# Performance work log

Measured on AMD Instinct MI355X. Metric: run time of the kernel, lower is better.

The kernel has to match this reference:

```python
import jax, jax.numpy as jnp
import numpy as np

N_E = 8192
E_DIM = 512
BETA = 0.25


def setup_inputs() -> dict:
    key = jax.random.key(0)
    k1, k2, k3, k4 = jax.random.split(key, 4)
    x = jax.random.normal(k1, (32, 512, E_DIM), dtype=jnp.float32)
    label = jax.random.randint(k2, (32, 512), 0, 100, dtype=jnp.int64)
    idx = jax.random.randint(k3, (32, 512), 0, 512, dtype=jnp.int64)
    # codebook initialized uniform(-1/n_e, 1/n_e) as in the torch module
    W = jax.random.uniform(k4, (N_E, E_DIM), dtype=jnp.float32,
                           minval=-1.0 / N_E, maxval=1.0 / N_E)
    return {"x": x, "label": label, "idx": idx, "W": W}


def reference(x, label, idx, W):
    # label/idx are unused in the forward math (mirrors the torch module)
    latent = x.reshape(-1, E_DIM)                        # [N, e_dim]
    # squared euclidean distances: ||z||^2 + ||c||^2 - 2 z c^T
    d = (jnp.sum(latent ** 2, axis=1, keepdims=True)
         + jnp.sum(W ** 2, axis=1)[None, :]
         - 2.0 * jnp.matmul(latent, W.T))                # [N, n_e]
    indices = jnp.argmin(d, axis=-1)                     # [N]
    x_q = W[indices].reshape(x.shape)                    # gather + reshape
    commitment_loss = jnp.mean((jax.lax.stop_gradient(x_q) - x) ** 2)
    loss = BETA * commitment_loss
    # straight-through estimator
    x_q = x + jax.lax.stop_gradient(x_q - x)
    indices = indices.reshape(x.shape[:-1])
    return x_q, loss, indices
```

## Files before the change

kernel.cpp:

```cpp
#include <hip/hip_runtime.h>
#include <cstdint>
#include <cstddef>

#define EDIM  512
#define NROWS 16384
#define NE    8192
#define XQSZ  (NROWS * EDIM)
#define NTILE 64
#define K3    1536

#define OFF_PART  0
#define OFF_Z     16384
#define OFF_C2    81920
#define OFF_KEYS  114688
#define OFF_TMIN  245760
#define OFF_CNT   4440064
#define OFF_LIST  4441088
#define OFF_XE    8635392
#define OFF_WE    58967040

typedef __attribute__((ext_vector_type(8)))  short          short8;
typedef __attribute__((ext_vector_type(16))) float          f32x16;
typedef __attribute__((ext_vector_type(4)))  unsigned short u16x4;

__device__ __forceinline__ float rownorm512(const float* __restrict__ p) {
#pragma clang fp contract(off)
    float S[4];
#pragma unroll
    for (int b = 0; b < 4; ++b) {
        const float* q = p + b * 128;
        float r[8];
#pragma unroll
        for (int j = 0; j < 8; ++j) { float v = q[j]; r[j] = v * v; }
        for (int i = 8; i < 128; i += 8) {
#pragma unroll
            for (int j = 0; j < 8; ++j) { float v = q[i + j]; r[j] = r[j] + v * v; }
        }
        S[b] = ((r[0] + r[1]) + (r[2] + r[3])) + ((r[4] + r[5]) + (r[6] + r[7]));
    }
    return (S[0] + S[1]) + (S[2] + S[3]);
}

__device__ __forceinline__ unsigned short f2bf(float f) {
    unsigned u = __float_as_uint(f);
    return (unsigned short)((u + 0x7FFFu + ((u >> 16) & 1u)) >> 16);
}
__device__ __forceinline__ float bf2f(unsigned short h) {
    return __uint_as_float(((unsigned)h) << 16);
}

__device__ __forceinline__ void split_group(const float* __restrict__ in,
        unsigned short* __restrict__ outp, int e) {
    int row = e >> 7;
    int d0  = (e & 127) << 2;
    float4 v = *(const float4*)(in + (size_t)row * EDIM + d0);
    float vv[4] = {v.x, v.y, v.z, v.w};
    u16x4 H, M, L;
#pragma unroll
    for (int i = 0; i < 4; ++i) {
        float f = vv[i];
        unsigned short h = f2bf(f);
        float r1 = f - bf2f(h);
        unsigned short m = f2bf(r1);
        float r2 = r1 - bf2f(m);
        L[i] = f2bf(r2); H[i] = h; M[i] = m;
    }
    unsigned short* o = outp + (size_t)row * K3 + d0;
    *(u16x4*)(o) = H; *(u16x4*)(o + EDIM) = M; *(u16x4*)(o + 2 * EDIM) = L;
}

__global__ __launch_bounds__(256) void k_prep(
        const float* __restrict__ x, const float* __restrict__ W,
        unsigned short* __restrict__ Xe, unsigned short* __restrict__ We,
        float* __restrict__ Z, float* __restrict__ c2) {
    const int bid = blockIdx.x, tid = threadIdx.x;
    if (bid < 8192) {
        split_group(x, Xe, bid * 256 + tid);
    } else if (bid < 12288) {
        split_group(W, We, (bid - 8192) * 256 + tid);
    } else if (bid < 12352) {
        const int row = (bid - 12288) * 256 + tid;
        Z[row] = rownorm512(x + (size_t)row * EDIM);
    } else {
        const int row = (bid - 12352) * 256 + tid;
        c2[row] = rownorm512(W + (size_t)row * EDIM);
    }
}

__device__ __forceinline__ void gld16(const void* g, void* l) {
    __builtin_amdgcn_global_load_lds((const __attribute__((address_space(1))) void*)g,
                                     (__attribute__((address_space(3))) void*)l, 16, 0, 0);
}

#define GBM 128
#define GBN 128
#define GBK 64

__global__ __launch_bounds__(256) void k_argmin_hi(
        const unsigned short* __restrict__ Xe, const unsigned short* __restrict__ We,
        const float* __restrict__ c2, unsigned* __restrict__ tmin) {
    __shared__ __align__(16) unsigned short At[GBM * GBK];
    __shared__ __align__(16) unsigned short Bt[GBN * GBK];
    __shared__ unsigned smin[GBM];
    __shared__ float cs[GBN];

    const int tid = threadIdx.x;
    const int lane = tid & 63, wid = tid >> 6;
    const int wr = wid >> 1, wc = wid & 1;

    const int bid = blockIdx.x;
    const int swz = (bid & 7) * 1024 + (bid >> 3);
    const int rowtile = swz & 127, codetile = swz >> 7;
    const int row0 = rowtile * GBM, code0 = codetile * GBN;

    if (tid < GBM) smin[tid] = 0xFFFFFFFFu;
    if (tid < GBN) cs[tid] = 4.0f + c2[code0 + tid];

    f32x16 acc[2][2];
#pragma unroll
    for (int i = 0; i < 2; ++i)
#pragma unroll
        for (int j = 0; j < 2; ++j)
#pragma unroll
            for (int r = 0; r < 16; ++r) acc[i][j][r] = 0.0f;

    size_t ga[4], gb[4];
#pragma unroll
    for (int i = 0; i < 4; ++i) {
        int chunk = i * 256 + tid;
        int row   = chunk >> 3;
        int kcs   = (chunk & 7) ^ (row & 7);
        ga[i] = (size_t)(row0 + row) * K3 + kcs * 8;
        gb[i] = (size_t)(code0 + row) * K3 + kcs * 8;
    }

    const int cb0 = wr * 64 + (lane & 31);
    const int xa0 = wc * 64 + (lane & 31);
    const int kh  = lane >> 5;
    const int sb  = cb0 & 7, sa = xa0 & 7;

    for (int kt = 0; kt < EDIM / GBK; ++kt) {
        const size_t ko = (size_t)kt * GBK;
#pragma unroll
        for (int i = 0; i < 4; ++i) {
            gld16(Xe + ga[i] + ko, (char*)At + i * 4096 + wid * 1024);
            gld16(We + gb[i] + ko, (char*)Bt + i * 4096 + wid * 1024);
        }
        __syncthreads();
#pragma unroll
        for (int ks = 0; ks < 4; ++ks) {
            const int ch = ks * 2 + kh;
            short8 c0 = *(const short8*)((const char*)Bt + cb0 * 128        + ((ch ^ sb) * 16));
            short8 c1 = *(const short8*)((const char*)Bt + (cb0 + 32) * 128 + ((ch ^ sb) * 16));
            short8 x0 = *(const short8*)((const char*)At + xa0 * 128        + ((ch ^ sa) * 16));
            short8 x1 = *(const short8*)((const char*)At + (xa0 + 32) * 128 + ((ch ^ sa) * 16));
            acc[0][0] = __builtin_amdgcn_mfma_f32_32x32x16_bf16(c0, x0, acc[0][0], 0, 0, 0);
            acc[0][1] = __builtin_amdgcn_mfma_f32_32x32x16_bf16(c0, x1, acc[0][1], 0, 0, 0);
            acc[1][0] = __builtin_amdgcn_mfma_f32_32x32x16_bf16(c1, x0, acc[1][0], 0, 0, 0);
            acc[1][1] = __builtin_amdgcn_mfma_f32_32x32x16_bf16(c1, x1, acc[1][1], 0, 0, 0);
        }
        __syncthreads();
    }

    const int kh4 = kh * 4;
#pragma unroll
    for (int nj = 0; nj < 2; ++nj) {
        float dmin = 3.4e38f;
#pragma unroll
        for (int mi = 0; mi < 2; ++mi) {
#pragma unroll
            for (int q = 0; q < 4; ++q) {
                const float4 cq = *(const float4*)&cs[wr * 64 + mi * 32 + q * 8 + kh4];
                dmin = fminf(dmin, fmaf(-2.0f, acc[mi][nj][q * 4 + 0], cq.x));
                dmin = fminf(dmin, fmaf(-2.0f, acc[mi][nj][q * 4 + 1], cq.y));
                dmin = fminf(dmin, fmaf(-2.0f, acc[mi][nj][q * 4 + 2], cq.z));
                dmin = fminf(dmin, fmaf(-2.0f, acc[mi][nj][q * 4 + 3], cq.w));
            }
        }
        const int xr = wc * 64 + nj * 32 + (lane & 31);
        atomicMin(&smin[xr], __float_as_uint(dmin));
    }
    __syncthreads();
    if (tid < GBM) tmin[codetile * NROWS + row0 + tid] = smin[tid];
}

__global__ __launch_bounds__(256) void k_select(
        const unsigned* __restrict__ tmin, const float* __restrict__ Z,
        int* __restrict__ cnt, int* __restrict__ list) {
    const int row = blockIdx.x * 256 + threadIdx.x;
    unsigned mn = 0xFFFFFFFFu;
    for (int t = 0; t < NTILE; ++t) {
        unsigned v = tmin[t * NROWS + row];
        if (v < mn) mn = v;
    }
    const float margin = 4.35e-5f * sqrtf(Z[row]) + 1.7e-4f;
    const float thr = __uint_as_float(mn) + margin;
    for (int t = 0; t < NTILE; ++t) {
        if (__uint_as_float(tmin[t * NROWS + row]) <= thr) {
            int p = atomicAdd(&cnt[t], 1);
            list[t * NROWS + p] = row;
        }
    }
}

__global__ __launch_bounds__(256) void k_rescore_mfma(
        const unsigned short* __restrict__ Xe, const unsigned short* __restrict__ We,
        const float* __restrict__ Z, const float* __restrict__ c2,
        const int* __restrict__ cnt, const int* __restrict__ list,
        unsigned long long* __restrict__ keys) {
    __shared__ __align__(16) unsigned short At[2][GBM * GBK];
    __shared__ __align__(16) unsigned short Bt[2][GBN * GBK];
    __shared__ int rl_s[GBM];
    __shared__ float Zs[GBM];
    __shared__ float cs2[GBN];

    const int tile = blockIdx.x;
    const int n = cnt[tile];
    if (n == 0) return;
    const int* rows = list + tile * NROWS;
    const int tid = threadIdx.x;
    const int lane = tid & 63, wid = tid >> 6;
    const int wr = wid >> 1, wc = wid & 1;
    const int code0 = tile * 128;

    if (tid < GBN) cs2[tid] = c2[code0 + tid];

    const int cb0 = wr * 64 + (lane & 31);
    const int xa0 = wc * 64 + (lane & 31);
    const int kh  = lane >> 5;
    const int kh4 = kh * 4;
    const int sb  = cb0 & 7, sa = xa0 & 7;

    size_t boff[4];
    int arow4[4], akcs4[4];
#pragma unroll
    for (int i = 0; i < 4; ++i) {
        int chunk = i * 256 + tid;
        int row   = chunk >> 3;
        int kcs   = (chunk & 7) ^ (row & 7);
        arow4[i] = row; akcs4[i] = kcs;
        boff[i] = (size_t)(code0 + row) * K3 + kcs * 8;
    }

#define RSTAGE(ss, bb) { \
        const int bt_ = (ss) >> 3, kc_ = (ss) & 7; \
        const int ao_ = (bt_ == 1 || bt_ == 2) ? EDIM : (bt_ == 4 ? 2 * EDIM : 0); \
        const int bo_ = (bt_ == 0 || bt_ == 2) ? EDIM : (bt_ == 3 ? 2 * EDIM : 0); \
        _Pragma("unroll") \
        for (int i_ = 0; i_ < 4; ++i_) { \
            gld16(Xe + aoff[i_] + ao_ + kc_ * GBK, (char*)At[bb] + i_ * 4096 + wid * 1024); \
            gld16(We + boff[i_] + bo_ + kc_ * GBK, (char*)Bt[bb] + i_ * 4096 + wid * 1024); \
        } }

#define RCOMP(bb) { \
        _Pragma("unroll") \
        for (int ks_ = 0; ks_ < 4; ++ks_) { \
            const int ch_ = ks_ * 2 + kh; \
            short8 cf0 = *(const short8*)((const char*)Bt[bb] + cb0 * 128        + ((ch_ ^ sb) * 16)); \
            short8 cf1 = *(const short8*)((const char*)Bt[bb] + (cb0 + 32) * 128 + ((ch_ ^ sb) * 16)); \
            short8 xf0 = *(const short8*)((const char*)At[bb] + xa0 * 128        + ((ch_ ^ sa) * 16)); \
            short8 xf1 = *(const short8*)((const char*)At[bb] + (xa0 + 32) * 128 + ((ch_ ^ sa) * 16)); \
            acc[0][0] = __builtin_amdgcn_mfma_f32_32x32x16_bf16(cf0, xf0, acc[0][0], 0, 0, 0); \
            acc[0][1] = __builtin_amdgcn_mfma_f32_32x32x16_bf16(cf0, xf1, acc[0][1], 0, 0, 0); \
            acc[1][0] = __builtin_amdgcn_mfma_f32_32x32x16_bf16(cf1, xf0, acc[1][0], 0, 0, 0); \
            acc[1][1] = __builtin_amdgcn_mfma_f32_32x32x16_bf16(cf1, xf1, acc[1][1], 0, 0, 0); \
        } }

    for (int chk = (int)blockIdx.y; chk * GBM < n; chk += 16) {
        __syncthreads();
        if (tid < GBM) {
            int ri = chk * GBM + tid;
            int r = rows[ri < n ? ri : 0];
            rl_s[tid] = r;
            Zs[tid] = Z[r];
        }
        __syncthreads();

        size_t aoff[4];
#pragma unroll
        for (int i = 0; i < 4; ++i)
            aoff[i] = (size_t)rl_s[arow4[i]] * K3 + akcs4[i] * 8;

        f32x16 acc[2][2];
#pragma unroll
        for (int i = 0; i < 2; ++i)
#pragma unroll
            for (int j = 0; j < 2; ++j)
#pragma unroll
                for (int r = 0; r < 16; ++r) acc[i][j][r] = 0.0f;

        RSTAGE(0, 0);
#pragma unroll 1
        for (int s = 0; s < 47; ++s) {
            RSTAGE(s + 1, (s + 1) & 1);
            asm volatile("s_waitcnt vmcnt(8)" ::: "memory");
            asm volatile("s_barrier" ::: "memory");
            RCOMP(s & 1);
            asm volatile("s_barrier" ::: "memory");
        }
        asm volatile("s_waitcnt vmcnt(0)" ::: "memory");
        asm volatile("s_barrier" ::: "memory");
        RCOMP(1);

#pragma unroll
        for (int nj = 0; nj < 2; ++nj) {
            const int xr = wc * 64 + nj * 32 + (lane & 31);
            const float Zr = Zs[xr];
            float dm = 3.4e38f; int jm = 0;
#pragma unroll
            for (int mi = 0; mi < 2; ++mi) {
#pragma unroll
                for (int q = 0; q < 4; ++q) {
                    const float4 cq = *(const float4*)&cs2[wr * 64 + mi * 32 + q * 8 + kh4];
                    const int jb = code0 + wr * 64 + mi * 32 + q * 8 + kh4;
                    { const float d = (Zr + cq.x) - 2.0f * acc[mi][nj][q * 4 + 0];
                      if (d < dm) { dm = d; jm = jb + 0; } }
                    { const float d = (Zr + cq.y) - 2.0f * acc[mi][nj][q * 4 + 1];
                      if (d < dm) { dm = d; jm = jb + 1; } }
                    { const float d = (Zr + cq.z) - 2.0f * acc[mi][nj][q * 4 + 2];
                      if (d < dm) { dm = d; jm = jb + 2; } }
                    { const float d = (Zr + cq.w) - 2.0f * acc[mi][nj][q * 4 + 3];
                      if (d < dm) { dm = d; jm = jb + 3; } }
                }
            }
            const unsigned long long k =
                (((unsigned long long)__float_as_uint(dm)) << 13) | (unsigned)jm;
            atomicMin(&keys[rl_s[xr]], k);
        }
    }
#undef RSTAGE
#undef RCOMP
}

__global__ __launch_bounds__(256) void k_gather(
        const float* __restrict__ x, const float* __restrict__ W,
        const unsigned long long* __restrict__ keys,
        float* __restrict__ out, double* __restrict__ part) {
    const int tid = threadIdx.x;
    const int row = blockIdx.x * 8 + (tid >> 5);
    const int c = tid & 31;
    const int idx = (int)(keys[row] & 0x1FFFull);

    const float* wrow = W + (size_t)idx * EDIM;
    const float* xrow = x + (size_t)row * EDIM;
    float* orow = out + (size_t)row * EDIM;

    double lsum = 0.0;
#pragma unroll
    for (int v = 0; v < 4; ++v) {
        const int d = c * 4 + v * 128;
        float4 xv = *(const float4*)(xrow + d);
        float4 wv = *(const float4*)(wrow + d);
        float t0 = wv.x - xv.x, t1 = wv.y - xv.y, t2 = wv.z - xv.z, t3 = wv.w - xv.w;
        float4 ov = { xv.x + t0, xv.y + t1, xv.z + t2, xv.w + t3 };
        *(float4*)(orow + d) = ov;
        lsum += (double)t0 * t0 + (double)t1 * t1 + (double)t2 * t2 + (double)t3 * t3;
    }
    if (c == 0) out[XQSZ + 1 + row] = (float)idx;

#pragma unroll
    for (int off = 32; off > 0; off >>= 1) lsum += __shfl_down(lsum, off, 64);
    __shared__ double pb[4];
    if ((tid & 63) == 0) pb[tid >> 6] = lsum;
    __syncthreads();
    if (tid == 0) part[blockIdx.x] = pb[0] + pb[1] + pb[2] + pb[3];
}

__global__ __launch_bounds__(256) void k_finalize(float* __restrict__ out,
        const double* __restrict__ part) {
    const int tid = threadIdx.x;
    double s = 0.0;
    for (int i = tid; i < 2048; i += 256) s += part[i];
#pragma unroll
    for (int off = 32; off > 0; off >>= 1) s += __shfl_down(s, off, 64);
    __shared__ double pb[4];
    if ((tid & 63) == 0) pb[tid >> 6] = s;
    __syncthreads();
    if (tid == 0) out[XQSZ] = (float)(0.25 * (pb[0] + pb[1] + pb[2] + pb[3]) / (double)XQSZ);
}

extern "C" void kernel_launch(void* const* d_in, const int* in_sizes, int n_in,
                              void* d_out, int out_size, void* d_ws, size_t ws_size,
                              hipStream_t stream) {
    const float* x = (const float*)d_in[0];
    const float* W = (const float*)d_in[3];
    float* out = (float*)d_out;
    char* ws = (char*)d_ws;

    double* part = (double*)(ws + OFF_PART);
    float* Z    = (float*)(ws + OFF_Z);
    float* c2   = (float*)(ws + OFF_C2);
    unsigned long long* keys = (unsigned long long*)(ws + OFF_KEYS);
    unsigned* tmin = (unsigned*)(ws + OFF_TMIN);
    int* cnt  = (int*)(ws + OFF_CNT);
    int* list = (int*)(ws + OFF_LIST);
    unsigned short* Xe = (unsigned short*)(ws + OFF_XE);
    unsigned short* We = (unsigned short*)(ws + OFF_WE);

    hipMemsetAsync(keys, 0xFF, NROWS * sizeof(unsigned long long), stream);
    hipMemsetAsync(cnt, 0, NTILE * sizeof(int), stream);
    k_prep<<<12384, 256, 0, stream>>>(x, W, Xe, We, Z, c2);
    k_argmin_hi<<<(NROWS / GBM) * (NE / GBN), 256, 0, stream>>>(Xe, We, c2, tmin);
    k_select<<<NROWS / 256, 256, 0, stream>>>(tmin, Z, cnt, list);
    k_rescore_mfma<<<dim3(NTILE, 16), 256, 0, stream>>>(Xe, We, Z, c2, cnt, list, keys);
    k_gather<<<NROWS / 8, 256, 0, stream>>>(x, W, keys, out, part);
    k_finalize<<<1, 256, 0, stream>>>(out, part);
}
```

Measured before the change: 567.3 us.

## Load rescore MFMA operands directly from global memory instead of LDS staging

The rescoring kernel no longer stages X and codebook tiles through double-buffered shared memory with async loads and barriers. Each lane now reads its bf16 fragments straight from global memory (relying on cache) and feeds them to the MFMAs in a fully unrolled loop. This removes the LDS footprint, the barriers and the staging instructions, which can raise occupancy. In exchange, each fragment is fetched redundantly by several waves through the cache, loads are strided and uncoalesced, and there is no explicit prefetch overlap.

```diff
diff --git a/kernel.cpp b/kernel.cpp
--- a/kernel.cpp
+++ b/kernel.cpp
@@ -208,8 +208,6 @@
         const float* __restrict__ Z, const float* __restrict__ c2,
         const int* __restrict__ cnt, const int* __restrict__ list,
         unsigned long long* __restrict__ keys) {
-    __shared__ __align__(16) unsigned short At[2][GBM * GBK];
-    __shared__ __align__(16) unsigned short Bt[2][GBN * GBK];
     __shared__ int rl_s[GBM];
     __shared__ float Zs[GBM];
     __shared__ float cs2[GBN];
@@ -229,42 +227,9 @@
     const int xa0 = wc * 64 + (lane & 31);
     const int kh  = lane >> 5;
     const int kh4 = kh * 4;
-    const int sb  = cb0 & 7, sa = xa0 & 7;
-
-    size_t boff[4];
-    int arow4[4], akcs4[4];
-#pragma unroll
-    for (int i = 0; i < 4; ++i) {
-        int chunk = i * 256 + tid;
-        int row   = chunk >> 3;
-        int kcs   = (chunk & 7) ^ (row & 7);
-        arow4[i] = row; akcs4[i] = kcs;
-        boff[i] = (size_t)(code0 + row) * K3 + kcs * 8;
-    }
-
-#define RSTAGE(ss, bb) { \
-        const int bt_ = (ss) >> 3, kc_ = (ss) & 7; \
-        const int ao_ = (bt_ == 1 || bt_ == 2) ? EDIM : (bt_ == 4 ? 2 * EDIM : 0); \
-        const int bo_ = (bt_ == 0 || bt_ == 2) ? EDIM : (bt_ == 3 ? 2 * EDIM : 0); \
-        _Pragma("unroll") \
-        for (int i_ = 0; i_ < 4; ++i_) { \
-            gld16(Xe + aoff[i_] + ao_ + kc_ * GBK, (char*)At[bb] + i_ * 4096 + wid * 1024); \
-            gld16(We + boff[i_] + bo_ + kc_ * GBK, (char*)Bt[bb] + i_ * 4096 + wid * 1024); \
-        } }
-
-#define RCOMP(bb) { \
-        _Pragma("unroll") \
-        for (int ks_ = 0; ks_ < 4; ++ks_) { \
-            const int ch_ = ks_ * 2 + kh; \
-            short8 cf0 = *(const short8*)((const char*)Bt[bb] + cb0 * 128        + ((ch_ ^ sb) * 16)); \
-            short8 cf1 = *(const short8*)((const char*)Bt[bb] + (cb0 + 32) * 128 + ((ch_ ^ sb) * 16)); \
-            short8 xf0 = *(const short8*)((const char*)At[bb] + xa0 * 128        + ((ch_ ^ sa) * 16)); \
-            short8 xf1 = *(const short8*)((const char*)At[bb] + (xa0 + 32) * 128 + ((ch_ ^ sa) * 16)); \
-            acc[0][0] = __builtin_amdgcn_mfma_f32_32x32x16_bf16(cf0, xf0, acc[0][0], 0, 0, 0); \
-            acc[0][1] = __builtin_amdgcn_mfma_f32_32x32x16_bf16(cf0, xf1, acc[0][1], 0, 0, 0); \
-            acc[1][0] = __builtin_amdgcn_mfma_f32_32x32x16_bf16(cf1, xf0, acc[1][0], 0, 0, 0); \
-            acc[1][1] = __builtin_amdgcn_mfma_f32_32x32x16_bf16(cf1, xf1, acc[1][1], 0, 0, 0); \
-        } }
+
+    const unsigned short* b0p = We + (size_t)(code0 + cb0) * K3;
+    const unsigned short* b1p = We + (size_t)(code0 + cb0 + 32) * K3;
 
     for (int chk = (int)blockIdx.y; chk * GBM < n; chk += 16) {
         __syncthreads();
@@ -276,10 +241,8 @@
         }
         __syncthreads();
 
-        size_t aoff[4];
-#pragma unroll
-        for (int i = 0; i < 4; ++i)
-            aoff[i] = (size_t)rl_s[arow4[i]] * K3 + akcs4[i] * 8;
+        const unsigned short* a0p = Xe + (size_t)rl_s[xa0] * K3;
+        const unsigned short* a1p = Xe + (size_t)rl_s[xa0 + 32] * K3;
 
         f32x16 acc[2][2];
 #pragma unroll
@@ -289,18 +252,26 @@
 #pragma unroll
                 for (int r = 0; r < 16; ++r) acc[i][j][r] = 0.0f;
 
-        RSTAGE(0, 0);
-#pragma unroll 1
-        for (int s = 0; s < 47; ++s) {
-            RSTAGE(s + 1, (s + 1) & 1);
-            asm volatile("s_waitcnt vmcnt(8)" ::: "memory");
-            asm volatile("s_barrier" ::: "memory");
-            RCOMP(s & 1);
-            asm volatile("s_barrier" ::: "memory");
-        }
-        asm volatile("s_waitcnt vmcnt(0)" ::: "memory");
-        asm volatile("s_barrier" ::: "memory");
-        RCOMP(1);
+#pragma unroll
+        for (int bt = 0; bt < 6; ++bt) {
+            const int ao = (bt == 1 || bt == 2) ? EDIM : (bt == 4 ? 2 * EDIM : 0);
+            const int bo = (bt == 0 || bt == 2) ? EDIM : (bt == 3 ? 2 * EDIM : 0);
+#pragma unroll
+            for (int kc = 0; kc < 8; ++kc) {
+#pragma unroll
+                for (int ks = 0; ks < 4; ++ks) {
+                    const int e  = (kc * 8 + ks * 2 + kh) * 8;
+                    short8 xf0 = *(const short8*)(a0p + ao + e);
+                    short8 xf1 = *(const short8*)(a1p + ao + e);
+                    short8 cf0 = *(const short8*)(b0p + bo + e);
+                    short8 cf1 = *(const short8*)(b1p + bo + e);
+                    acc[0][0] = __builtin_amdgcn_mfma_f32_32x32x16_bf16(cf0, xf0, acc[0][0], 0, 0, 0);
+                    acc[0][1] = __builtin_amdgcn_mfma_f32_32x32x16_bf16(cf0, xf1, acc[0][1], 0, 0, 0);
+                    acc[1][0] = __builtin_amdgcn_mfma_f32_32x32x16_bf16(cf1, xf0, acc[1][0], 0, 0, 0);
+                    acc[1][1] = __builtin_amdgcn_mfma_f32_32x32x16_bf16(cf1, xf1, acc[1][1], 0, 0, 0);
+                }
+            }
+        }
 
 #pragma unroll
         for (int nj = 0; nj < 2; ++nj) {
@@ -328,8 +299,6 @@
             atomicMin(&keys[rl_s[xr]], k);
         }
     }
-#undef RSTAGE
-#undef RCOMP
 }
 
 __global__ __launch_bounds__(256) void k_gather(
```

New measurement: 1.028 ms. +81.3%, slower.
